# Kernel optimization log

Hardware: AMD Instinct MI355X
Metric: run time of the kernel (lower is better)

The kernel has to match this reference:

```python
import jax, jax.numpy as jnp
import numpy as np

S, N_SUB, E_SUB = 64, 1024, 16384       # subgraphs, nodes/subgraph, edges/subgraph
N, E = 65536, 1048576                   # global nodes / edges
F_IN, NHID, NCLS, HEADS = 128, 128, 64, 2
RATIO = 0.5
K = int(np.ceil(RATIO * N_SUB))         # SAGPooling keeps K=512 nodes


def setup_inputs() -> dict:
    key = jax.random.key(0)
    ks = jax.random.split(key, 12)
    def lin(k, i, o):
        return jax.random.normal(k, (i, o), jnp.float32) / np.sqrt(i).astype(np.float32)
    return {
        'sub_x': jax.random.normal(ks[0], (S, N_SUB, F_IN), jnp.float32),
        'sub_edge_index': jax.random.randint(ks[1], (S, 2, E_SUB), 0, N_SUB, jnp.int32),
        'sub_orig_idx': jax.random.randint(ks[2], (S, N_SUB), 0, N, jnp.int32),
        'edge_index': jax.random.randint(ks[3], (2, E), 0, N, jnp.int32),
        'W1': lin(ks[4], F_IN, NHID), 'b1': jnp.zeros((NHID,), jnp.float32),
        'W2': lin(ks[5], NHID, NHID), 'b2': jnp.zeros((NHID,), jnp.float32),
        'Wp': lin(ks[6], NHID, 1), 'bp': jnp.zeros((1,), jnp.float32),
        'Wsc': lin(ks[7], NHID, NHID), 'bsc': jnp.zeros((NHID,), jnp.float32),
        'Wqkv': lin(ks[8], 2 * NHID, 6 * NHID), 'bqkv': jnp.zeros((6 * NHID,), jnp.float32),
        'Wo': lin(ks[9], 2 * NHID, 2 * NHID), 'bo': jnp.zeros((2 * NHID,), jnp.float32),
        'Wf': lin(ks[10], 3 * NHID, NCLS), 'bf': jnp.zeros((NCLS,), jnp.float32),
    }


def gcn(x, src, dst, ew, W, b, n):
    """PyG GCNConv: sym-normalized aggregation with self-loops; ew masks invalid edges."""
    h = x @ W
    deg = jax.ops.segment_sum(ew, dst, num_segments=n) + 1.0  # +1 self-loop
    dinv = jax.lax.rsqrt(deg)
    coef = dinv[src] * dinv[dst] * ew
    agg = jax.ops.segment_sum(h[src] * coef[:, None], dst, num_segments=n)
    return agg + h * (dinv * dinv)[:, None] + b


def _forward(sub_x, W1, b1, W2, b2, Wp, bp, Wsc, bsc, Wqkv, bqkv, Wo, bo, Wf, bf,
             sub_edge_index, sub_orig_idx, edge_index):
    dt = sub_x.dtype

    def cacos(x, ei):  # one subgraph: [N_SUB,F], [2,E_SUB]
        src, dst = ei[0], ei[1]
        ew1 = jnp.ones((E_SUB,), dt)
        x1 = jax.nn.relu(gcn(x, src, dst, ew1, W1, b1, N_SUB))
        x2 = jax.nn.relu(gcn(x1, src, dst, ew1, W2, b2, N_SUB))
        # SAGPooling on x1: GCN scorer -> top-k -> tanh gate
        score = gcn(x1, src, dst, ew1, Wp, bp, N_SUB)[:, 0]
        top_s, perm = jax.lax.top_k(score, K)
        x_pool = x1[perm] * jnp.tanh(top_s)[:, None]
        # remap edges to pooled indexing; invalid edges get weight 0
        pos = jnp.full((N_SUB,), -1, jnp.int32).at[perm].set(jnp.arange(K, dtype=jnp.int32))
        valid = (pos[src] >= 0) & (pos[dst] >= 0)
        psrc = jnp.where(valid, pos[src], 0)
        pdst = jnp.where(valid, pos[dst], 0)
        ew2 = valid.astype(dt)
        emb1 = jnp.concatenate([x_pool.max(0), x_pool.mean(0)])  # [2*NHID]
        x_sub = jax.nn.relu(gcn(x_pool, psrc, pdst, ew2, Wsc, bsc, K))
        emb2 = jnp.concatenate([x_sub.max(0), x_sub.mean(0)])
        return x2, emb1 + emb2

    node_embs, sub_embs = jax.vmap(cacos)(sub_x, sub_edge_index)  # [S,N_SUB,NHID], [S,2*NHID]

    # multi-head self-attention over subgraph embeddings (seq_len = 1 per the torch reshape)
    HD = (2 * NHID) // HEADS
    qkv = (sub_embs @ Wqkv + bqkv).reshape(S, 1, 3, HEADS, HD).transpose(2, 0, 3, 1, 4)
    q, k, v = qkv[0], qkv[1], qkv[2]                      # [S,H,1,HD]
    attn = jax.nn.softmax(jnp.einsum('shqd,shkd->shqk', q, k) / np.sqrt(HD).astype(np.float32), axis=-1)
    o = jnp.einsum('shqk,shkd->shqd', attn, v).transpose(0, 2, 1, 3).reshape(S, 1, 2 * NHID)
    att = (o @ Wo + bo)[:, 0]                             # [S, 2*NHID]

    # scatter-add per-node embeddings + broadcast subgraph embedding into global buffer
    combined = jnp.concatenate(
        [node_embs, jnp.broadcast_to(att[:, None, :], (S, N_SUB, 2 * NHID))], axis=-1)
    global_emb = jnp.zeros((N, 3 * NHID), dt).at[sub_orig_idx.reshape(-1)].add(
        combined.reshape(-1, 3 * NHID))

    logits = gcn(global_emb, edge_index[0], edge_index[1], jnp.ones((E,), dt), Wf, bf, N)
    return jax.nn.log_softmax(logits, axis=-1), global_emb


def reference(sub_x, sub_edge_index, sub_orig_idx, edge_index, W1, b1, W2, b2, Wp, bp,
              Wsc, bsc, Wqkv, bqkv, Wo, bo, Wf, bf):
    return _forward(sub_x, W1, b1, W2, b2, Wp, bp, Wsc, bsc, Wqkv, bqkv, Wo, bo, Wf, bf,
                    sub_edge_index, sub_orig_idx, edge_index)
```

## Files before the change

### kernel.cpp

```cpp
#include <hip/hip_runtime.h>
#include <math.h>

#define S     64
#define NSUB  1024
#define ESUB  16384
#define NG    65536
#define EG    1048576
#define NH    128
#define KSEL  512
#define BCAP  20480

__global__ __launch_bounds__(1024) void k_csr_sub(const int* __restrict__ sei,
        const int* __restrict__ sorig, int* __restrict__ rowptr, int* __restrict__ col,
        float* __restrict__ dinv, int* __restrict__ cntR) {
    int b = blockIdx.x, t = threadIdx.x;
    if (b >= 64) {
        int r = (b - 64) * 1024 + t;
        atomicAdd(&cntR[sorig[r]], 1);
        return;
    }
    __shared__ int sh[1024];
    __shared__ int curL[1024];
    int s = b;
    curL[t] = 0;
    __syncthreads();
    const int* dstp = sei + s * 2 * ESUB + ESUB;
    #pragma unroll
    for (int k = 0; k < 16; k++) atomicAdd(&curL[dstp[k * 1024 + t]], 1);
    __syncthreads();
    int v = curL[t];
    sh[t] = v;
    __syncthreads();
    for (int off = 1; off < 1024; off <<= 1) {
        int add = (t >= off) ? sh[t - off] : 0;
        __syncthreads();
        sh[t] += add;
        __syncthreads();
    }
    int incl = sh[t];
    int excl = incl - v;
    rowptr[s * (NSUB + 1) + t] = excl;
    dinv[s * NSUB + t] = rsqrtf((float)(v + 1));
    if (t == 1023) rowptr[s * (NSUB + 1) + NSUB] = incl;
    curL[t] = s * ESUB + excl;
    __syncthreads();
    const int* srcp = sei + s * 2 * ESUB;
    #pragma unroll
    for (int k = 0; k < 16; k++) {
        int e = k * 1024 + t;
        int src = srcp[e];
        int dst = dstp[e];
        int p = atomicAdd(&curL[dst], 1);
        col[p] = src;
    }
}

__global__ __launch_bounds__(1024) void k_scanR(const int* __restrict__ cnt,
        int* __restrict__ rowptr, int* __restrict__ cur, int* __restrict__ bcur) {
    __shared__ int sh[1024];
    __shared__ int wsum[16];
    __shared__ int sboff;
    int b = blockIdx.x, t = threadIdx.x;
    if (b == 0 && t < 64) bcur[t] = t * BCAP;
    int pre = 0;
    for (int i = t; i < b * 1024; i += 1024) pre += cnt[i];
    #pragma unroll
    for (int o = 32; o > 0; o >>= 1) pre += __shfl_xor(pre, o, 64);
    if ((t & 63) == 0) wsum[t >> 6] = pre;
    __syncthreads();
    if (t == 0) {
        int r = 0;
        #pragma unroll
        for (int i = 0; i < 16; i++) r += wsum[i];
        sboff = r;
    }
    int v = cnt[b * 1024 + t];
    sh[t] = v;
    __syncthreads();
    for (int off = 1; off < 1024; off <<= 1) {
        int add = (t >= off) ? sh[t - off] : 0;
        __syncthreads();
        sh[t] += add;
        __syncthreads();
    }
    int base = sboff;
    int r = base + sh[t] - v;
    int idx = b * 1024 + t;
    rowptr[idx] = r;
    cur[idx] = r;
    if (b == 63 && t == 1023) rowptr[NG] = base + sh[t];
}

__global__ void k_fillR(const int* __restrict__ orig, int* __restrict__ cur,
                        int* __restrict__ rowlist, int* __restrict__ posR) {
    int r = blockIdx.x * 256 + threadIdx.x;
    int p = atomicAdd(&cur[orig[r]], 1);
    rowlist[p] = r;
    posR[r] = p;
}

template<int KDIM, int NCOL>
__global__ __launch_bounds__(256) void k_matmul(const float* __restrict__ X,
        const float* __restrict__ W, float* __restrict__ Y) {
    __shared__ float As[16][72];
    __shared__ float Bs[16][72];
    int t = threadIdx.x;
    int row0 = blockIdx.x * 64;
    int col0 = blockIdx.y * 64;
    int tr = t >> 4, tc = t & 15;
    float acc[4][4] = {};
    for (int k0 = 0; k0 < KDIM; k0 += 16) {
        {
            int r = t >> 2, kq = t & 3;
            float4 v = *(const float4*)&X[(size_t)(row0 + r) * KDIM + k0 + kq * 4];
            As[kq * 4 + 0][r] = v.x; As[kq * 4 + 1][r] = v.y;
            As[kq * 4 + 2][r] = v.z; As[kq * 4 + 3][r] = v.w;
        }
        {
            int k = t >> 4, cq = t & 15;
            float4 v = *(const float4*)&W[(size_t)(k0 + k) * NCOL + col0 + cq * 4];
            *(float4*)&Bs[k][cq * 4] = v;
        }
        __syncthreads();
        #pragma unroll
        for (int k = 0; k < 16; k++) {
            float a0 = As[k][tr * 4 + 0], a1 = As[k][tr * 4 + 1];
            float a2 = As[k][tr * 4 + 2], a3 = As[k][tr * 4 + 3];
            float b0 = Bs[k][tc * 4 + 0], b1 = Bs[k][tc * 4 + 1];
            float b2 = Bs[k][tc * 4 + 2], b3 = Bs[k][tc * 4 + 3];
            acc[0][0] += a0 * b0; acc[0][1] += a0 * b1; acc[0][2] += a0 * b2; acc[0][3] += a0 * b3;
            acc[1][0] += a1 * b0; acc[1][1] += a1 * b1; acc[1][2] += a1 * b2; acc[1][3] += a1 * b3;
            acc[2][0] += a2 * b0; acc[2][1] += a2 * b1; acc[2][2] += a2 * b2; acc[2][3] += a2 * b3;
            acc[3][0] += a3 * b0; acc[3][1] += a3 * b1; acc[3][2] += a3 * b2; acc[3][3] += a3 * b3;
        }
        __syncthreads();
    }
    #pragma unroll
    for (int i = 0; i < 4; i++) {
        float4 v = { acc[i][0], acc[i][1], acc[i][2], acc[i][3] };
        *(float4*)&Y[(size_t)(row0 + tr * 4 + i) * NCOL + col0 + tc * 4] = v;
    }
}

template<bool SCORE, bool SCATTER>
__global__ __launch_bounds__(256) void k_agg128(const float4* __restrict__ h,
        const float* __restrict__ dinv, const int* __restrict__ rowptr,
        const int* __restrict__ col, const float* __restrict__ bias,
        const float* __restrict__ Wp, const int* __restrict__ posR,
        float4* __restrict__ out, float* __restrict__ scoreh) {
    int b = blockIdx.x;
    int s = b & 63;
    int chunk = b >> 6;
    int t = threadIdx.x;
    int nl = chunk * 8 + (t >> 5);
    int f4 = t & 31;
    const int* rp = rowptr + s * (NSUB + 1);
    int st = rp[nl], en = rp[nl + 1];
    const int* cl = col + s * ESUB;
    const float* dv = dinv + s * NSUB;
    float4 acc = {0.f, 0.f, 0.f, 0.f};
    for (int p = st; p < en; p++) {
        int src = cl[p];
        float d = dv[src];
        float4 hv = h[((size_t)(s * NSUB + src)) * 32 + f4];
        acc.x += hv.x * d; acc.y += hv.y * d; acc.z += hv.z * d; acc.w += hv.w * d;
    }
    size_t node = (size_t)s * NSUB + nl;
    float dn = dv[nl];
    float dn2 = dn * dn;
    float4 hs = h[node * 32 + f4];
    float4 bb = ((const float4*)bias)[f4];
    float4 r;
    r.x = fmaxf(acc.x * dn + hs.x * dn2 + bb.x, 0.f);
    r.y = fmaxf(acc.y * dn + hs.y * dn2 + bb.y, 0.f);
    r.z = fmaxf(acc.z * dn + hs.z * dn2 + bb.z, 0.f);
    r.w = fmaxf(acc.w * dn + hs.w * dn2 + bb.w, 0.f);
    size_t orow = SCATTER ? (size_t)posR[node] : node;
    out[orow * 32 + f4] = r;
    if (SCORE) {
        float4 wp = ((const float4*)Wp)[f4];
        float p = r.x * wp.x + r.y * wp.y + r.z * wp.z + r.w * wp.w;
        #pragma unroll
        for (int o = 16; o > 0; o >>= 1) p += __shfl_xor(p, o, 32);
        if (f4 == 0) scoreh[node] = p;
    }
}

__global__ void k_score_agg(const float* __restrict__ sh, const float* __restrict__ dinv,
                            const int* __restrict__ rowptr, const int* __restrict__ col,
                            const float* __restrict__ bp, float* __restrict__ score) {
    int n = blockIdx.x * 256 + threadIdx.x;
    int s = n >> 10, nl = n & (NSUB - 1);
    const int* rp = rowptr + s * (NSUB + 1);
    const int* cl = col + s * ESUB;
    const float* dv = dinv + s * NSUB;
    int st = rp[nl], en = rp[nl + 1];
    float acc = 0.f;
    for (int p = st; p < en; p++) {
        int src = cl[p];
        acc += sh[s * NSUB + src] * dv[src];
    }
    float dn = dv[nl];
    score[n] = acc * dn + sh[n] * dn * dn + bp[0];
}

__global__ __launch_bounds__(512) void k_topk(const float* __restrict__ score,
        int* __restrict__ perm, float* __restrict__ gate, int* __restrict__ posmap) {
    __shared__ float sv[1024];
    __shared__ int   si[1024];
    int s = blockIdx.x, t = threadIdx.x;
    for (int i = t; i < 1024; i += 512) {
        sv[i] = score[s * NSUB + i];
        si[i] = i;
        posmap[s * NSUB + i] = -1;
    }
    __syncthreads();
    for (int k = 2; k <= 1024; k <<= 1) {
        for (int j = k >> 1; j > 0; j >>= 1) {
            for (int b = t; b < 1024; b += 512) {
                int ixj = b ^ j;
                if (ixj > b) {
                    bool desc = ((b & k) == 0);
                    bool sw = desc ? (sv[b] < sv[ixj]) : (sv[b] > sv[ixj]);
                    if (sw) {
                        float tv = sv[b]; sv[b] = sv[ixj]; sv[ixj] = tv;
                        int ti = si[b]; si[b] = si[ixj]; si[ixj] = ti;
                    }
                }
            }
            __syncthreads();
        }
    }
    if (t < KSEL) {
        perm[s * KSEL + t] = si[t];
        gate[s * KSEL + t] = tanhf(sv[t]);
        posmap[s * NSUB + si[t]] = t;
    }
}

__global__ __launch_bounds__(256) void k_pool(const float4* __restrict__ x1,
        const int* __restrict__ perm, const float* __restrict__ gate,
        const int* __restrict__ posmap, const int* __restrict__ rowptr,
        const int* __restrict__ col, float* __restrict__ dinv2,
        float4* __restrict__ xpool) {
    int t = threadIdx.x;
    int i = blockIdx.x * 8 + (t >> 5);
    int lane = t & 31;
    int s = i >> 9;
    int n = perm[i];
    const int* rp = rowptr + s * (NSUB + 1);
    const int* cl = col + s * ESUB;
    int st = rp[n], en = rp[n + 1];
    int c = 0;
    for (int p = st + lane; p < en; p += 32) c += (posmap[s * NSUB + cl[p]] >= 0) ? 1 : 0;
    #pragma unroll
    for (int o = 16; o > 0; o >>= 1) c += __shfl_xor(c, o, 32);
    if (lane == 0) dinv2[i] = rsqrtf((float)(c + 1));
    float g = gate[i];
    float4 v = x1[((size_t)(s * NSUB + n)) * 32 + lane];
    v.x *= g; v.y *= g; v.z *= g; v.w *= g;
    xpool[(size_t)i * 32 + lane] = v;
}

__global__ __launch_bounds__(1024) void k_emb(const float* __restrict__ X,
        float* __restrict__ out) {
    __shared__ float red[4][256];
    int s = blockIdx.x, t = threadIdx.x;
    int sl = t >> 8, f = t & 255;
    const float* base = X + (size_t)s * KSEL * NH;
    float r;
    if (f < NH) {
        r = -INFINITY;
        for (int i = sl * 128; i < sl * 128 + 128; i++) r = fmaxf(r, base[i * NH + f]);
    } else {
        r = 0.f;
        for (int i = sl * 128; i < sl * 128 + 128; i++) r += base[i * NH + (f - NH)];
    }
    red[sl][f] = r;
    __syncthreads();
    if (sl == 0) {
        float a = red[0][f], b = red[1][f], c = red[2][f], d = red[3][f];
        float v = (f < NH) ? fmaxf(fmaxf(a, b), fmaxf(c, d)) : (a + b + c + d) * (1.f / KSEL);
        out[s * 256 + f] = v;
    }
}

__global__ __launch_bounds__(1024) void k_emb_attn(const float* __restrict__ X,
        const float* __restrict__ subemb, const float* __restrict__ Wqkv,
        const float* __restrict__ bqkv, const float* __restrict__ Wo,
        const float* __restrict__ bo, const float* __restrict__ Wf,
        float* __restrict__ att, float* __restrict__ AW) {
    __shared__ float red[4][256];
    __shared__ float se[256], t1[256], av[256];
    int s = blockIdx.x, t = threadIdx.x;
    int sl = t >> 8, f = t & 255;
    const float* base = X + (size_t)s * KSEL * NH;
    float r;
    if (f < NH) {
        r = -INFINITY;
        for (int i = sl * 128; i < sl * 128 + 128; i++) r = fmaxf(r, base[i * NH + f]);
    } else {
        r = 0.f;
        for (int i = sl * 128; i < sl * 128 + 128; i++) r += base[i * NH + (f - NH)];
    }
    red[sl][f] = r;
    __syncthreads();
    if (sl == 0) {
        float a = red[0][f], b = red[1][f], c = red[2][f], d = red[3][f];
        float v = (f < NH) ? fmaxf(fmaxf(a, b), fmaxf(c, d)) : (a + b + c + d) * (1.f / KSEL);
        se[f] = subemb[s * 256 + f] + v;
    }
    __syncthreads();
    if (sl == 0) {
        float acc = bqkv[512 + f];
        for (int k = 0; k < 256; k++) acc += se[k] * Wqkv[(size_t)k * 768 + 512 + f];
        t1[f] = acc;
    }
    __syncthreads();
    if (sl == 0) {
        float a2 = bo[f];
        for (int k = 0; k < 256; k++) a2 += t1[k] * Wo[(size_t)k * 256 + f];
        att[s * 256 + f] = a2;
        av[f] = a2;
    }
    __syncthreads();
    if (sl == 0 && f < 64) {
        float acc = 0.f;
        for (int k = 0; k < 256; k++) acc += av[k] * Wf[(size_t)(NH + k) * 64 + f];
        AW[s * 64 + f] = acc;
    }
}

__global__ __launch_bounds__(256) void k_agg_pool(const float4* __restrict__ hp,
        const float* __restrict__ dinv2, const int* __restrict__ perm,
        const int* __restrict__ posmap, const int* __restrict__ rowptr,
        const int* __restrict__ col, const float* __restrict__ bsc,
        float4* __restrict__ xsub) {
    int b = blockIdx.x;
    int s = b & 63;
    int chunk = b >> 6;
    int t = threadIdx.x;
    int il = chunk * 8 + (t >> 5);
    int f4 = t & 31;
    int i = s * KSEL + il;
    int n = perm[i];
    const int* rp = rowptr + s * (NSUB + 1);
    const int* cl = col + s * ESUB;
    int st = rp[n], en = rp[n + 1];
    float4 acc = {0.f, 0.f, 0.f, 0.f};
    for (int p = st; p < en; p++) {
        int j = posmap[s * NSUB + cl[p]];
        if (j >= 0) {
            float d = dinv2[s * KSEL + j];
            float4 hv = hp[((size_t)(s * KSEL + j)) * 32 + f4];
            acc.x += hv.x * d; acc.y += hv.y * d; acc.z += hv.z * d; acc.w += hv.w * d;
        }
    }
    float dn = dinv2[i];
    float dn2 = dn * dn;
    float4 hs = hp[(size_t)i * 32 + f4];
    float4 bb = ((const float4*)bsc)[f4];
    float4 r;
    r.x = fmaxf(acc.x * dn + hs.x * dn2 + bb.x, 0.f);
    r.y = fmaxf(acc.y * dn + hs.y * dn2 + bb.y, 0.f);
    r.z = fmaxf(acc.z * dn + hs.z * dn2 + bb.z, 0.f);
    r.w = fmaxf(acc.w * dn + hs.w * dn2 + bb.w, 0.f);
    xsub[(size_t)i * 32 + f4] = r;
}

__global__ __launch_bounds__(384) void k_gather(const float4* __restrict__ x2s,
        const float4* __restrict__ att, const int* __restrict__ rowptrR,
        const int* __restrict__ rowlist, float4* __restrict__ gemb) {
    int t = threadIdx.x;
    int g = blockIdx.x * 4 + (t / 96);
    int lane = t % 96;
    int st = rowptrR[g], en = rowptrR[g + 1];
    float4 acc = {0.f, 0.f, 0.f, 0.f};
    if (lane < 32) {
        for (int p = st; p < en; p++) {
            float4 v = x2s[(size_t)p * 32 + lane];
            acc.x += v.x; acc.y += v.y; acc.z += v.z; acc.w += v.w;
        }
    } else {
        for (int p = st; p < en; p++) {
            int sub = rowlist[p] >> 10;
            float4 v = att[(size_t)sub * 64 + (lane - 32)];
            acc.x += v.x; acc.y += v.y; acc.z += v.z; acc.w += v.w;
        }
    }
    gemb[(size_t)g * 96 + lane] = acc;
}

__global__ __launch_bounds__(256) void k_x2w(const float* __restrict__ X,
        const float* __restrict__ W, const int* __restrict__ rowlist,
        const float* __restrict__ AW, float* __restrict__ Y) {
    __shared__ float As[16][72];
    __shared__ float Bs[16][72];
    int t = threadIdx.x;
    int row0 = blockIdx.x * 64;
    int tr = t >> 4, tc = t & 15;
    float acc[4][4] = {};
    for (int k0 = 0; k0 < 128; k0 += 16) {
        {   int r = t >> 2, kq = t & 3;
            float4 v = *(const float4*)&X[(size_t)(row0 + r) * 128 + k0 + kq * 4];
            As[kq * 4 + 0][r] = v.x; As[kq * 4 + 1][r] = v.y;
            As[kq * 4 + 2][r] = v.z; As[kq * 4 + 3][r] = v.w;
        }
        {   int k = t >> 4, cq = t & 15;
            float4 v = *(const float4*)&W[(size_t)(k0 + k) * 64 + cq * 4];
            *(float4*)&Bs[k][cq * 4] = v;
        }
        __syncthreads();
        #pragma unroll
        for (int k = 0; k < 16; k++) {
            float a0 = As[k][tr * 4 + 0], a1 = As[k][tr * 4 + 1];
            float a2 = As[k][tr * 4 + 2], a3 = As[k][tr * 4 + 3];
            float b0 = Bs[k][tc * 4 + 0], b1 = Bs[k][tc * 4 + 1];
            float b2 = Bs[k][tc * 4 + 2], b3 = Bs[k][tc * 4 + 3];
            acc[0][0] += a0 * b0; acc[0][1] += a0 * b1; acc[0][2] += a0 * b2; acc[0][3] += a0 * b3;
            acc[1][0] += a1 * b0; acc[1][1] += a1 * b1; acc[1][2] += a1 * b2; acc[1][3] += a1 * b3;
            acc[2][0] += a2 * b0; acc[2][1] += a2 * b1; acc[2][2] += a2 * b2; acc[2][3] += a2 * b3;
            acc[3][0] += a3 * b0; acc[3][1] += a3 * b1; acc[3][2] += a3 * b2; acc[3][3] += a3 * b3;
        }
        __syncthreads();
    }
    #pragma unroll
    for (int i = 0; i < 4; i++) {
        int rr = row0 + tr * 4 + i;
        int sub = rowlist[rr] >> 10;
        const float4 aw = *(const float4*)&AW[(size_t)sub * 64 + tc * 4];
        float4 v = { acc[i][0] + aw.x, acc[i][1] + aw.y, acc[i][2] + aw.z, acc[i][3] + aw.w };
        *(float4*)&Y[(size_t)rr * 64 + tc * 4] = v;
    }
}

__global__ __launch_bounds__(256) void k_gatherH(const float4* __restrict__ X2Ws,
        const int* __restrict__ rowptrR, float4* __restrict__ hf) {
    int t = threadIdx.x;
    int g = blockIdx.x * 16 + (t >> 4);
    int f4 = t & 15;
    int st = rowptrR[g], en = rowptrR[g + 1];
    float4 acc = {0.f, 0.f, 0.f, 0.f};
    for (int p = st; p < en; p++) {
        float4 a = X2Ws[(size_t)p * 16 + f4];
        acc.x += a.x; acc.y += a.y; acc.z += a.z; acc.w += a.w;
    }
    hf[(size_t)g * 16 + f4] = acc;
}

__global__ __launch_bounds__(256) void k_binN(const int* __restrict__ gei,
        int* __restrict__ bcur, int* __restrict__ ebin) {
    __shared__ int lh[64];
    __shared__ int lbase[64];
    int t = threadIdx.x;
    if (t < 64) lh[t] = 0;
    __syncthreads();
    int e0 = blockIdx.x * 8192;
    #pragma unroll 8
    for (int k = 0; k < 32; k++) {
        int d = gei[EG + e0 + k * 256 + t];
        atomicAdd(&lh[d >> 10], 1);
    }
    __syncthreads();
    if (t < 64) {
        lbase[t] = atomicAdd(&bcur[t], lh[t]);
        lh[t] = 0;
    }
    __syncthreads();
    #pragma unroll 4
    for (int k = 0; k < 32; k++) {
        int idx = e0 + k * 256 + t;
        int d = gei[EG + idx];
        int src = gei[idx];
        int bb = d >> 10;
        int pos = lbase[bb] + atomicAdd(&lh[bb], 1);
        ebin[pos] = src | ((d & 1023) << 16);
    }
}

__global__ __launch_bounds__(1024) void k_fillB3(const int* __restrict__ ebin,
        const int* __restrict__ bcur, int* __restrict__ rowptrN,
        float* __restrict__ dinvN, int* __restrict__ colN) {
    __shared__ int sh[1024];
    __shared__ int curL[1024];
    __shared__ int sbase;
    int b = blockIdx.x, t = threadIdx.x;
    if (t == 0) {
        int run = 0;
        for (int i = 0; i < b; i++) run += bcur[i] - i * BCAP;
        sbase = run;
    }
    curL[t] = 0;
    __syncthreads();
    int st = b * BCAP, en = bcur[b];
    for (int i = st + t; i < en; i += 1024) atomicAdd(&curL[ebin[i] >> 16], 1);
    __syncthreads();
    int v = curL[t];
    sh[t] = v;
    __syncthreads();
    for (int off = 1; off < 1024; off <<= 1) {
        int add = (t >= off) ? sh[t - off] : 0;
        __syncthreads();
        sh[t] += add;
        __syncthreads();
    }
    int incl = sh[t];
    int excl = incl - v;
    int base = sbase;
    rowptrN[(b << 10) + t] = base + excl;
    dinvN[(b << 10) + t] = rsqrtf((float)(v + 1));
    if (b == 63 && t == 1023) rowptrN[NG] = base + incl;
    curL[t] = base + excl;
    __syncthreads();
    for (int i = st + t; i < en; i += 1024) {
        int packed = ebin[i];
        int p = atomicAdd(&curL[packed >> 16], 1);
        colN[p] = packed & 0xFFFF;
    }
}

__global__ __launch_bounds__(256) void k_final(const float4* __restrict__ hf,
        const float* __restrict__ dinvN, const int* __restrict__ rowptr,
        const int* __restrict__ col, const float* __restrict__ bfb,
        float4* __restrict__ out) {
    int t = threadIdx.x;
    int n = blockIdx.x * 16 + (t >> 4);
    int f4 = t & 15;
    int st = rowptr[n], en = rowptr[n + 1];
    float4 acc = {0.f, 0.f, 0.f, 0.f};
    for (int p = st; p < en; p++) {
        int src = col[p];
        float d = dinvN[src];
        float4 hv = hf[(size_t)src * 16 + f4];
        acc.x += hv.x * d; acc.y += hv.y * d; acc.z += hv.z * d; acc.w += hv.w * d;
    }
    float dn = dinvN[n];
    float dn2 = dn * dn;
    float4 hs = hf[(size_t)n * 16 + f4];
    float4 bb = ((const float4*)bfb)[f4];
    float4 x;
    x.x = acc.x * dn + hs.x * dn2 + bb.x;
    x.y = acc.y * dn + hs.y * dn2 + bb.y;
    x.z = acc.z * dn + hs.z * dn2 + bb.z;
    x.w = acc.w * dn + hs.w * dn2 + bb.w;
    float m = fmaxf(fmaxf(x.x, x.y), fmaxf(x.z, x.w));
    for (int o = 1; o < 16; o <<= 1) m = fmaxf(m, __shfl_xor(m, o, 64));
    float ssum = expf(x.x - m) + expf(x.y - m) + expf(x.z - m) + expf(x.w - m);
    for (int o = 1; o < 16; o <<= 1) ssum += __shfl_xor(ssum, o, 64);
    float lz = m + logf(ssum);
    float4 r = { x.x - lz, x.y - lz, x.z - lz, x.w - lz };
    out[(size_t)n * 16 + f4] = r;
}

extern "C" void kernel_launch(void* const* d_in, const int* in_sizes, int n_in,
                              void* d_out, int out_size, void* d_ws, size_t ws_size,
                              hipStream_t stream) {
    const float* sub_x = (const float*)d_in[0];
    const int*   sei   = (const int*)d_in[1];
    const int*   sorig = (const int*)d_in[2];
    const int*   gei   = (const int*)d_in[3];
    const float *W1 = (const float*)d_in[4],  *b1  = (const float*)d_in[5];
    const float *W2 = (const float*)d_in[6],  *b2  = (const float*)d_in[7];
    const float *Wp = (const float*)d_in[8],  *bp  = (const float*)d_in[9];
    const float *Wsc = (const float*)d_in[10], *bsc = (const float*)d_in[11];
    const float *Wqkv = (const float*)d_in[12], *bqkv = (const float*)d_in[13];
    const float *Wo = (const float*)d_in[14], *bo  = (const float*)d_in[15];
    const float *Wf = (const float*)d_in[16], *bfb = (const float*)d_in[17];

    float* out0 = (float*)d_out;
    float* gemb = (float*)d_out + (size_t)NG * 64;

    char* w = (char*)d_ws;
    size_t off = 0;
    auto alloc = [&](size_t nbytes) -> void* {
        off = (off + 255) & ~(size_t)255;
        void* p = w + off;
        off += nbytes;
        return p;
    };
    int*   bcur    = (int*)alloc(64 * 4);
    float* AW      = (float*)alloc((size_t)S * 64 * 4);
    float* dinv    = (float*)alloc((size_t)NG * 4);
    float* scoreh  = (float*)alloc((size_t)NG * 4);
    float* score   = (float*)alloc((size_t)NG * 4);
    float* gate    = (float*)alloc((size_t)S * KSEL * 4);
    float* dinv2   = (float*)alloc((size_t)S * KSEL * 4);
    float* subemb  = (float*)alloc((size_t)S * 256 * 4);
    float* att     = (float*)alloc((size_t)S * 256 * 4);
    int*   perm    = (int*)alloc((size_t)S * KSEL * 4);
    int*   posmap  = (int*)alloc((size_t)NG * 4);
    int*   cur_sub = (int*)alloc((size_t)NG * 4);
    int*   rowptr_s= (int*)alloc((size_t)(NG + 64) * 4);
    int*   col_sub = (int*)alloc((size_t)EG * 4);
    int*   rowptrR = (int*)alloc((size_t)(NG + 64) * 4);
    int*   cntR    = (int*)alloc((size_t)NG * 4);
    int*   rowlist = (int*)alloc((size_t)NG * 4);
    int*   posR    = (int*)alloc((size_t)NG * 4);
    float* x1      = (float*)alloc((size_t)NG * NH * 4);
    float* x2s     = (float*)alloc((size_t)NG * NH * 4);
    float* hbuf    = (float*)alloc((size_t)NG * NH * 4);
    float* xpool   = (float*)alloc((size_t)S * KSEL * NH * 4);
    float* xsub    = x1;
    float* hf      = hbuf;
    float* dinvN   = dinv;
    float* X2Ws    = x1;
    int*   curR    = cur_sub;
    int*   rowptrN = rowptr_s;
    int*   colN    = col_sub;
    int*   ebin    = (int*)xpool;

    hipMemsetAsync(cntR, 0, (size_t)NG * 4, stream);

    k_csr_sub<<<128, 1024, 0, stream>>>(sei, sorig, rowptr_s, col_sub, dinv, cntR);
    k_scanR<<<64, 1024, 0, stream>>>(cntR, rowptrR, curR, bcur);
    k_fillR<<<NG / 256, 256, 0, stream>>>(sorig, curR, rowlist, posR);

    k_matmul<128, 128><<<dim3(NG / 64, 2), 256, 0, stream>>>(sub_x, W1, hbuf);
    k_agg128<true, false><<<8192, 256, 0, stream>>>((const float4*)hbuf, dinv, rowptr_s,
                                                    col_sub, b1, Wp, nullptr, (float4*)x1, scoreh);
    k_matmul<128, 128><<<dim3(NG / 64, 2), 256, 0, stream>>>(x1, W2, hbuf);
    k_agg128<false, true><<<8192, 256, 0, stream>>>((const float4*)hbuf, dinv, rowptr_s,
                                                    col_sub, b2, nullptr, posR, (float4*)x2s, nullptr);
    k_score_agg<<<NG / 256, 256, 0, stream>>>(scoreh, dinv, rowptr_s, col_sub, bp, score);
    k_topk<<<S, 512, 0, stream>>>(score, perm, gate, posmap);
    k_pool<<<(S * KSEL) / 8, 256, 0, stream>>>((const float4*)x1, perm, gate, posmap,
                                               rowptr_s, col_sub, dinv2, (float4*)xpool);
    k_emb<<<S, 1024, 0, stream>>>(xpool, subemb);
    k_matmul<128, 128><<<dim3((S * KSEL) / 64, 2), 256, 0, stream>>>(xpool, Wsc, hbuf);
    k_agg_pool<<<4096, 256, 0, stream>>>((const float4*)hbuf, dinv2, perm, posmap,
                                         rowptr_s, col_sub, bsc, (float4*)xsub);
    k_emb_attn<<<S, 1024, 0, stream>>>(xsub, subemb, Wqkv, bqkv, Wo, bo, Wf, att, AW);

    k_binN<<<EG / 8192, 256, 0, stream>>>(gei, bcur, ebin);
    k_fillB3<<<64, 1024, 0, stream>>>(ebin, bcur, rowptrN, dinvN, colN);

    k_gather<<<NG / 4, 384, 0, stream>>>((const float4*)x2s, (const float4*)att,
                                         rowptrR, rowlist, (float4*)gemb);
    k_x2w<<<NG / 64, 256, 0, stream>>>(x2s, Wf, rowlist, AW, X2Ws);
    k_gatherH<<<NG / 16, 256, 0, stream>>>((const float4*)X2Ws, rowptrR, (float4*)hf);

    k_final<<<NG / 16, 256, 0, stream>>>((const float4*)hf, dinvN, rowptrN, colN, bfb, (float4*)out0);

    (void)in_sizes; (void)n_in; (void)out_size; (void)ws_size;
}
```

Before: 720.7 us.

## Merge independent kernels into shared launches via block-index partitioning

Several independent kernels are merged into single launches that split work by block index: the layer-2 matmul with score aggregation, pooled aggregation with global edge binning, embedding attention with CSR fill, and gather with the x2·Wf matmul. The bcur counter is now zeroed by the existing memset instead of set by k_scanR, and offsets are computed from counts. This cuts launch count and lets small, low-occupancy kernels overlap with larger ones. In exchange, heterogeneous blocks share one launch configuration, and the gather path is reshaped to 256-thread blocks with one warp handling all three segments.

```diff
diff --git a/kernel.cpp b/kernel.cpp
--- a/kernel.cpp
+++ b/kernel.cpp
@@ -56,12 +56,11 @@
 }
 
 __global__ __launch_bounds__(1024) void k_scanR(const int* __restrict__ cnt,
-        int* __restrict__ rowptr, int* __restrict__ cur, int* __restrict__ bcur) {
+        int* __restrict__ rowptr, int* __restrict__ cur) {
     __shared__ int sh[1024];
     __shared__ int wsum[16];
     __shared__ int sboff;
     int b = blockIdx.x, t = threadIdx.x;
-    if (b == 0 && t < 64) bcur[t] = t * BCAP;
     int pre = 0;
     for (int i = t; i < b * 1024; i += 1024) pre += cnt[i];
     #pragma unroll
@@ -110,14 +109,12 @@
     int tr = t >> 4, tc = t & 15;
     float acc[4][4] = {};
     for (int k0 = 0; k0 < KDIM; k0 += 16) {
-        {
-            int r = t >> 2, kq = t & 3;
+        {   int r = t >> 2, kq = t & 3;
             float4 v = *(const float4*)&X[(size_t)(row0 + r) * KDIM + k0 + kq * 4];
             As[kq * 4 + 0][r] = v.x; As[kq * 4 + 1][r] = v.y;
             As[kq * 4 + 2][r] = v.z; As[kq * 4 + 3][r] = v.w;
         }
-        {
-            int k = t >> 4, cq = t & 15;
+        {   int k = t >> 4, cq = t & 15;
             float4 v = *(const float4*)&W[(size_t)(k0 + k) * NCOL + col0 + cq * 4];
             *(float4*)&Bs[k][cq * 4] = v;
         }
@@ -139,6 +136,65 @@
     for (int i = 0; i < 4; i++) {
         float4 v = { acc[i][0], acc[i][1], acc[i][2], acc[i][3] };
         *(float4*)&Y[(size_t)(row0 + tr * 4 + i) * NCOL + col0 + tc * 4] = v;
+    }
+}
+
+__global__ __launch_bounds__(256) void k_mm2s(const float* __restrict__ X,
+        const float* __restrict__ W, float* __restrict__ Y,
+        const float* __restrict__ sh, const float* __restrict__ dinv,
+        const int* __restrict__ rowptr, const int* __restrict__ col,
+        const float* __restrict__ bp, float* __restrict__ score) {
+    int t = threadIdx.x;
+    if (blockIdx.x >= 2048) {
+        int n = (blockIdx.x - 2048) * 256 + t;
+        int s = n >> 10, nl = n & (NSUB - 1);
+        const int* rp = rowptr + s * (NSUB + 1);
+        const int* cl = col + s * ESUB;
+        const float* dv = dinv + s * NSUB;
+        int st = rp[nl], en = rp[nl + 1];
+        float acc = 0.f;
+        for (int p = st; p < en; p++) {
+            int src = cl[p];
+            acc += sh[s * NSUB + src] * dv[src];
+        }
+        float dn = dv[nl];
+        score[n] = acc * dn + sh[n] * dn * dn + bp[0];
+        return;
+    }
+    __shared__ float As[16][72];
+    __shared__ float Bs[16][72];
+    int row0 = (blockIdx.x & 1023) * 64;
+    int col0 = (blockIdx.x >> 10) * 64;
+    int tr = t >> 4, tc = t & 15;
+    float acc[4][4] = {};
+    for (int k0 = 0; k0 < 128; k0 += 16) {
+        {   int r = t >> 2, kq = t & 3;
+            float4 v = *(const float4*)&X[(size_t)(row0 + r) * 128 + k0 + kq * 4];
+            As[kq * 4 + 0][r] = v.x; As[kq * 4 + 1][r] = v.y;
+            As[kq * 4 + 2][r] = v.z; As[kq * 4 + 3][r] = v.w;
+        }
+        {   int k = t >> 4, cq = t & 15;
+            float4 v = *(const float4*)&W[(size_t)(k0 + k) * 128 + col0 + cq * 4];
+            *(float4*)&Bs[k][cq * 4] = v;
+        }
+        __syncthreads();
+        #pragma unroll
+        for (int k = 0; k < 16; k++) {
+            float a0 = As[k][tr * 4 + 0], a1 = As[k][tr * 4 + 1];
+            float a2 = As[k][tr * 4 + 2], a3 = As[k][tr * 4 + 3];
+            float b0 = Bs[k][tc * 4 + 0], b1 = Bs[k][tc * 4 + 1];
+            float b2 = Bs[k][tc * 4 + 2], b3 = Bs[k][tc * 4 + 3];
+            acc[0][0] += a0 * b0; acc[0][1] += a0 * b1; acc[0][2] += a0 * b2; acc[0][3] += a0 * b3;
+            acc[1][0] += a1 * b0; acc[1][1] += a1 * b1; acc[1][2] += a1 * b2; acc[1][3] += a1 * b3;
+            acc[2][0] += a2 * b0; acc[2][1] += a2 * b1; acc[2][2] += a2 * b2; acc[2][3] += a2 * b3;
+            acc[3][0] += a3 * b0; acc[3][1] += a3 * b1; acc[3][2] += a3 * b2; acc[3][3] += a3 * b3;
+        }
+        __syncthreads();
+    }
+    #pragma unroll
+    for (int i = 0; i < 4; i++) {
+        float4 v = { acc[i][0], acc[i][1], acc[i][2], acc[i][3] };
+        *(float4*)&Y[(size_t)(row0 + tr * 4 + i) * 128 + col0 + tc * 4] = v;
     }
 }
 
@@ -186,24 +242,6 @@
     }
 }
 
-__global__ void k_score_agg(const float* __restrict__ sh, const float* __restrict__ dinv,
-                            const int* __restrict__ rowptr, const int* __restrict__ col,
-                            const float* __restrict__ bp, float* __restrict__ score) {
-    int n = blockIdx.x * 256 + threadIdx.x;
-    int s = n >> 10, nl = n & (NSUB - 1);
-    const int* rp = rowptr + s * (NSUB + 1);
-    const int* cl = col + s * ESUB;
-    const float* dv = dinv + s * NSUB;
-    int st = rp[nl], en = rp[nl + 1];
-    float acc = 0.f;
-    for (int p = st; p < en; p++) {
-        int src = cl[p];
-        acc += sh[s * NSUB + src] * dv[src];
-    }
-    float dn = dv[nl];
-    score[n] = acc * dn + sh[n] * dn * dn + bp[0];
-}
-
 __global__ __launch_bounds__(512) void k_topk(const float* __restrict__ score,
         int* __restrict__ perm, float* __restrict__ gate, int* __restrict__ posmap) {
     __shared__ float sv[1024];
@@ -285,61 +323,44 @@
     }
 }
 
-__global__ __launch_bounds__(1024) void k_emb_attn(const float* __restrict__ X,
-        const float* __restrict__ subemb, const float* __restrict__ Wqkv,
-        const float* __restrict__ bqkv, const float* __restrict__ Wo,
-        const float* __restrict__ bo, const float* __restrict__ Wf,
-        float* __restrict__ att, float* __restrict__ AW) {
-    __shared__ float red[4][256];
-    __shared__ float se[256], t1[256], av[256];
-    int s = blockIdx.x, t = threadIdx.x;
-    int sl = t >> 8, f = t & 255;
-    const float* base = X + (size_t)s * KSEL * NH;
-    float r;
-    if (f < NH) {
-        r = -INFINITY;
-        for (int i = sl * 128; i < sl * 128 + 128; i++) r = fmaxf(r, base[i * NH + f]);
-    } else {
-        r = 0.f;
-        for (int i = sl * 128; i < sl * 128 + 128; i++) r += base[i * NH + (f - NH)];
-    }
-    red[sl][f] = r;
-    __syncthreads();
-    if (sl == 0) {
-        float a = red[0][f], b = red[1][f], c = red[2][f], d = red[3][f];
-        float v = (f < NH) ? fmaxf(fmaxf(a, b), fmaxf(c, d)) : (a + b + c + d) * (1.f / KSEL);
-        se[f] = subemb[s * 256 + f] + v;
-    }
-    __syncthreads();
-    if (sl == 0) {
-        float acc = bqkv[512 + f];
-        for (int k = 0; k < 256; k++) acc += se[k] * Wqkv[(size_t)k * 768 + 512 + f];
-        t1[f] = acc;
-    }
-    __syncthreads();
-    if (sl == 0) {
-        float a2 = bo[f];
-        for (int k = 0; k < 256; k++) a2 += t1[k] * Wo[(size_t)k * 256 + f];
-        att[s * 256 + f] = a2;
-        av[f] = a2;
-    }
-    __syncthreads();
-    if (sl == 0 && f < 64) {
-        float acc = 0.f;
-        for (int k = 0; k < 256; k++) acc += av[k] * Wf[(size_t)(NH + k) * 64 + f];
-        AW[s * 64 + f] = acc;
-    }
-}
-
-__global__ __launch_bounds__(256) void k_agg_pool(const float4* __restrict__ hp,
+__global__ __launch_bounds__(256) void k_aggp_bin(const float4* __restrict__ hp,
         const float* __restrict__ dinv2, const int* __restrict__ perm,
         const int* __restrict__ posmap, const int* __restrict__ rowptr,
         const int* __restrict__ col, const float* __restrict__ bsc,
-        float4* __restrict__ xsub) {
+        float4* __restrict__ xsub,
+        const int* __restrict__ gei, int* __restrict__ bcur, int* __restrict__ ebin) {
+    int t = threadIdx.x;
+    if (blockIdx.x >= 4096) {
+        __shared__ int lh[64];
+        __shared__ int lbase[64];
+        if (t < 64) lh[t] = 0;
+        __syncthreads();
+        int e0 = (blockIdx.x - 4096) * 8192;
+        #pragma unroll 8
+        for (int k = 0; k < 32; k++) {
+            int d = gei[EG + e0 + k * 256 + t];
+            atomicAdd(&lh[d >> 10], 1);
+        }
+        __syncthreads();
+        if (t < 64) {
+            lbase[t] = t * BCAP + atomicAdd(&bcur[t], lh[t]);
+            lh[t] = 0;
+        }
+        __syncthreads();
+        #pragma unroll 4
+        for (int k = 0; k < 32; k++) {
+            int idx = e0 + k * 256 + t;
+            int d = gei[EG + idx];
+            int src = gei[idx];
+            int bb = d >> 10;
+            int pos = lbase[bb] + atomicAdd(&lh[bb], 1);
+            ebin[pos] = src | ((d & 1023) << 16);
+        }
+        return;
+    }
     int b = blockIdx.x;
     int s = b & 63;
     int chunk = b >> 6;
-    int t = threadIdx.x;
     int il = chunk * 8 + (t >> 5);
     int f4 = t & 31;
     int i = s * KSEL + il;
@@ -368,36 +389,122 @@
     xsub[(size_t)i * 32 + f4] = r;
 }
 
-__global__ __launch_bounds__(384) void k_gather(const float4* __restrict__ x2s,
+__global__ __launch_bounds__(1024) void k_ea_fb(const float* __restrict__ X,
+        const float* __restrict__ subemb, const float* __restrict__ Wqkv,
+        const float* __restrict__ bqkv, const float* __restrict__ Wo,
+        const float* __restrict__ bo, const float* __restrict__ Wf,
+        float* __restrict__ att, float* __restrict__ AW,
+        const int* __restrict__ ebin, const int* __restrict__ bcur,
+        int* __restrict__ rowptrN, float* __restrict__ dinvN, int* __restrict__ colN) {
+    int t = threadIdx.x;
+    if (blockIdx.x >= 64) {
+        __shared__ int sh2[1024];
+        __shared__ int curL[1024];
+        __shared__ int sbase;
+        int b = blockIdx.x - 64;
+        if (t == 0) {
+            int run = 0;
+            for (int i = 0; i < b; i++) run += bcur[i];
+            sbase = run;
+        }
+        curL[t] = 0;
+        __syncthreads();
+        int st = b * BCAP, en = st + bcur[b];
+        for (int i = st + t; i < en; i += 1024) atomicAdd(&curL[ebin[i] >> 16], 1);
+        __syncthreads();
+        int v = curL[t];
+        sh2[t] = v;
+        __syncthreads();
+        for (int off = 1; off < 1024; off <<= 1) {
+            int add = (t >= off) ? sh2[t - off] : 0;
+            __syncthreads();
+            sh2[t] += add;
+            __syncthreads();
+        }
+        int incl = sh2[t];
+        int excl = incl - v;
+        int base = sbase;
+        rowptrN[(b << 10) + t] = base + excl;
+        dinvN[(b << 10) + t] = rsqrtf((float)(v + 1));
+        if (b == 63 && t == 1023) rowptrN[NG] = base + incl;
+        curL[t] = base + excl;
+        __syncthreads();
+        for (int i = st + t; i < en; i += 1024) {
+            int packed = ebin[i];
+            int p = atomicAdd(&curL[packed >> 16], 1);
+            colN[p] = packed & 0xFFFF;
+        }
+        return;
+    }
+    __shared__ float red[4][256];
+    __shared__ float se[256], t1[256], av[256];
+    int s = blockIdx.x;
+    int sl = t >> 8, f = t & 255;
+    const float* base = X + (size_t)s * KSEL * NH;
+    float r;
+    if (f < NH) {
+        r = -INFINITY;
+        for (int i = sl * 128; i < sl * 128 + 128; i++) r = fmaxf(r, base[i * NH + f]);
+    } else {
+        r = 0.f;
+        for (int i = sl * 128; i < sl * 128 + 128; i++) r += base[i * NH + (f - NH)];
+    }
+    red[sl][f] = r;
+    __syncthreads();
+    if (sl == 0) {
+        float a = red[0][f], b = red[1][f], c = red[2][f], d = red[3][f];
+        float v = (f < NH) ? fmaxf(fmaxf(a, b), fmaxf(c, d)) : (a + b + c + d) * (1.f / KSEL);
+        se[f] = subemb[s * 256 + f] + v;
+    }
+    __syncthreads();
+    if (sl == 0) {
+        float acc = bqkv[512 + f];
+        for (int k = 0; k < 256; k++) acc += se[k] * Wqkv[(size_t)k * 768 + 512 + f];
+        t1[f] = acc;
+    }
+    __syncthreads();
+    if (sl == 0) {
+        float a2 = bo[f];
+        for (int k = 0; k < 256; k++) a2 += t1[k] * Wo[(size_t)k * 256 + f];
+        att[s * 256 + f] = a2;
+        av[f] = a2;
+    }
+    __syncthreads();
+    if (sl == 0 && f < 64) {
+        float acc = 0.f;
+        for (int k = 0; k < 256; k++) acc += av[k] * Wf[(size_t)(NH + k) * 64 + f];
+        AW[s * 64 + f] = acc;
+    }
+}
+
+__global__ __launch_bounds__(256) void k_gx(const float4* __restrict__ x2s,
         const float4* __restrict__ att, const int* __restrict__ rowptrR,
-        const int* __restrict__ rowlist, float4* __restrict__ gemb) {
-    int t = threadIdx.x;
-    int g = blockIdx.x * 4 + (t / 96);
-    int lane = t % 96;
-    int st = rowptrR[g], en = rowptrR[g + 1];
-    float4 acc = {0.f, 0.f, 0.f, 0.f};
-    if (lane < 32) {
+        const int* __restrict__ rowlist, float4* __restrict__ gemb,
+        const float* __restrict__ X, const float* __restrict__ W,
+        const float* __restrict__ AW, float* __restrict__ Y) {
+    int t = threadIdx.x;
+    if (blockIdx.x < NG / 8) {
+        int g = blockIdx.x * 8 + (t >> 5);
+        int lane = t & 31;
+        int st = rowptrR[g], en = rowptrR[g + 1];
+        float4 a0 = {0.f,0.f,0.f,0.f}, a1 = {0.f,0.f,0.f,0.f}, a2 = {0.f,0.f,0.f,0.f};
         for (int p = st; p < en; p++) {
             float4 v = x2s[(size_t)p * 32 + lane];
-            acc.x += v.x; acc.y += v.y; acc.z += v.z; acc.w += v.w;
-        }
-    } else {
-        for (int p = st; p < en; p++) {
+            a0.x += v.x; a0.y += v.y; a0.z += v.z; a0.w += v.w;
             int sub = rowlist[p] >> 10;
-            float4 v = att[(size_t)sub * 64 + (lane - 32)];
-            acc.x += v.x; acc.y += v.y; acc.z += v.z; acc.w += v.w;
-        }
-    }
-    gemb[(size_t)g * 96 + lane] = acc;
-}
-
-__global__ __launch_bounds__(256) void k_x2w(const float* __restrict__ X,
-        const float* __restrict__ W, const int* __restrict__ rowlist,
-        const float* __restrict__ AW, float* __restrict__ Y) {
+            float4 w1 = att[(size_t)sub * 64 + lane];
+            float4 w2 = att[(size_t)sub * 64 + 32 + lane];
+            a1.x += w1.x; a1.y += w1.y; a1.z += w1.z; a1.w += w1.w;
+            a2.x += w2.x; a2.y += w2.y; a2.z += w2.z; a2.w += w2.w;
+        }
+        gemb[(size_t)g * 96 + lane]      = a0;
+        gemb[(size_t)g * 96 + 32 + lane] = a1;
+        gemb[(size_t)g * 96 + 64 + lane] = a2;
+        return;
+    }
     __shared__ float As[16][72];
     __shared__ float Bs[16][72];
-    int t = threadIdx.x;
-    int row0 = blockIdx.x * 64;
+    int row0 = (blockIdx.x - NG / 8) * 64;
     int tr = t >> 4, tc = t & 15;
     float acc[4][4] = {};
     for (int k0 = 0; k0 < 128; k0 += 16) {
@@ -446,77 +553,6 @@
         acc.x += a.x; acc.y += a.y; acc.z += a.z; acc.w += a.w;
     }
     hf[(size_t)g * 16 + f4] = acc;
-}
-
-__global__ __launch_bounds__(256) void k_binN(const int* __restrict__ gei,
-        int* __restrict__ bcur, int* __restrict__ ebin) {
-    __shared__ int lh[64];
-    __shared__ int lbase[64];
-    int t = threadIdx.x;
-    if (t < 64) lh[t] = 0;
-    __syncthreads();
-    int e0 = blockIdx.x * 8192;
-    #pragma unroll 8
-    for (int k = 0; k < 32; k++) {
-        int d = gei[EG + e0 + k * 256 + t];
-        atomicAdd(&lh[d >> 10], 1);
-    }
-    __syncthreads();
-    if (t < 64) {
-        lbase[t] = atomicAdd(&bcur[t], lh[t]);
-        lh[t] = 0;
-    }
-    __syncthreads();
-    #pragma unroll 4
-    for (int k = 0; k < 32; k++) {
-        int idx = e0 + k * 256 + t;
-        int d = gei[EG + idx];
-        int src = gei[idx];
-        int bb = d >> 10;
-        int pos = lbase[bb] + atomicAdd(&lh[bb], 1);
-        ebin[pos] = src | ((d & 1023) << 16);
-    }
-}
-
-__global__ __launch_bounds__(1024) void k_fillB3(const int* __restrict__ ebin,
-        const int* __restrict__ bcur, int* __restrict__ rowptrN,
-        float* __restrict__ dinvN, int* __restrict__ colN) {
-    __shared__ int sh[1024];
-    __shared__ int curL[1024];
-    __shared__ int sbase;
-    int b = blockIdx.x, t = threadIdx.x;
-    if (t == 0) {
-        int run = 0;
-        for (int i = 0; i < b; i++) run += bcur[i] - i * BCAP;
-        sbase = run;
-    }
-    curL[t] = 0;
-    __syncthreads();
-    int st = b * BCAP, en = bcur[b];
-    for (int i = st + t; i < en; i += 1024) atomicAdd(&curL[ebin[i] >> 16], 1);
-    __syncthreads();
-    int v = curL[t];
-    sh[t] = v;
-    __syncthreads();
-    for (int off = 1; off < 1024; off <<= 1) {
-        int add = (t >= off) ? sh[t - off] : 0;
-        __syncthreads();
-        sh[t] += add;
-        __syncthreads();
-    }
-    int incl = sh[t];
-    int excl = incl - v;
-    int base = sbase;
-    rowptrN[(b << 10) + t] = base + excl;
-    dinvN[(b << 10) + t] = rsqrtf((float)(v + 1));
-    if (b == 63 && t == 1023) rowptrN[NG] = base + incl;
-    curL[t] = base + excl;
-    __syncthreads();
-    for (int i = st + t; i < en; i += 1024) {
-        int packed = ebin[i];
-        int p = atomicAdd(&curL[packed >> 16], 1);
-        colN[p] = packed & 0xFFFF;
-    }
 }
 
 __global__ __launch_bounds__(256) void k_final(const float4* __restrict__ hf,
@@ -579,6 +615,7 @@
         return p;
     };
     int*   bcur    = (int*)alloc(64 * 4);
+    int*   cntR    = (int*)alloc((size_t)NG * 4);
     float* AW      = (float*)alloc((size_t)S * 64 * 4);
     float* dinv    = (float*)alloc((size_t)NG * 4);
     float* scoreh  = (float*)alloc((size_t)NG * 4);
@@ -593,7 +630,6 @@
     int*   rowptr_s= (int*)alloc((size_t)(NG + 64) * 4);
     int*   col_sub = (int*)alloc((size_t)EG * 4);
     int*   rowptrR = (int*)alloc((size_t)(NG + 64) * 4);
-    int*   cntR    = (int*)alloc((size_t)NG * 4);
     int*   rowlist = (int*)alloc((size_t)NG * 4);
     int*   posR    = (int*)alloc((size_t)NG * 4);
     float* x1      = (float*)alloc((size_t)NG * NH * 4);
@@ -609,34 +645,32 @@
     int*   colN    = col_sub;
     int*   ebin    = (int*)xpool;
 
-    hipMemsetAsync(cntR, 0, (size_t)NG * 4, stream);
+    hipMemsetAsync(bcur, 0, 256 + (size_t)NG * 4, stream);
 
     k_csr_sub<<<128, 1024, 0, stream>>>(sei, sorig, rowptr_s, col_sub, dinv, cntR);
-    k_scanR<<<64, 1024, 0, stream>>>(cntR, rowptrR, curR, bcur);
+    k_scanR<<<64, 1024, 0, stream>>>(cntR, rowptrR, curR);
     k_fillR<<<NG / 256, 256, 0, stream>>>(sorig, curR, rowlist, posR);
 
     k_matmul<128, 128><<<dim3(NG / 64, 2), 256, 0, stream>>>(sub_x, W1, hbuf);
     k_agg128<true, false><<<8192, 256, 0, stream>>>((const float4*)hbuf, dinv, rowptr_s,
                                                     col_sub, b1, Wp, nullptr, (float4*)x1, scoreh);
-    k_matmul<128, 128><<<dim3(NG / 64, 2), 256, 0, stream>>>(x1, W2, hbuf);
+    k_mm2s<<<2048 + NG / 256, 256, 0, stream>>>(x1, W2, hbuf,
+                                                scoreh, dinv, rowptr_s, col_sub, bp, score);
     k_agg128<false, true><<<8192, 256, 0, stream>>>((const float4*)hbuf, dinv, rowptr_s,
                                                     col_sub, b2, nullptr, posR, (float4*)x2s, nullptr);
-    k_score_agg<<<NG / 256, 256, 0, stream>>>(scoreh, dinv, rowptr_s, col_sub, bp, score);
     k_topk<<<S, 512, 0, stream>>>(score, perm, gate, posmap);
     k_pool<<<(S * KSEL) / 8, 256, 0, stream>>>((const float4*)x1, perm, gate, posmap,
                                                rowptr_s, col_sub, dinv2, (float4*)xpool);
     k_emb<<<S, 1024, 0, stream>>>(xpool, subemb);
     k_matmul<128, 128><<<dim3((S * KSEL) / 64, 2), 256, 0, stream>>>(xpool, Wsc, hbuf);
-    k_agg_pool<<<4096, 256, 0, stream>>>((const float4*)hbuf, dinv2, perm, posmap,
-                                         rowptr_s, col_sub, bsc, (float4*)xsub);
-    k_emb_attn<<<S, 1024, 0, stream>>>(xsub, subemb, Wqkv, bqkv, Wo, bo, Wf, att, AW);
-
-    k_binN<<<EG / 8192, 256, 0, stream>>>(gei, bcur, ebin);
-    k_fillB3<<<64, 1024, 0, stream>>>(ebin, bcur, rowptrN, dinvN, colN);
-
-    k_gather<<<NG / 4, 384, 0, stream>>>((const float4*)x2s, (const float4*)att,
-                                         rowptrR, rowlist, (float4*)gemb);
-    k_x2w<<<NG / 64, 256, 0, stream>>>(x2s, Wf, rowlist, AW, X2Ws);
+    k_aggp_bin<<<4096 + EG / 8192, 256, 0, stream>>>((const float4*)hbuf, dinv2, perm, posmap,
+                                                     rowptr_s, col_sub, bsc, (float4*)xsub,
+                                                     gei, bcur, ebin);
+    k_ea_fb<<<128, 1024, 0, stream>>>(xsub, subemb, Wqkv, bqkv, Wo, bo, Wf, att, AW,
+                                      ebin, bcur, rowptrN, dinvN, colN);
+    k_gx<<<NG / 8 + NG / 64, 256, 0, stream>>>((const float4*)x2s, (const float4*)att,
+                                               rowptrR, rowlist, (float4*)gemb,
+                                               x2s, Wf, AW, X2Ws);
     k_gatherH<<<NG / 16, 256, 0, stream>>>((const float4*)X2Ws, rowptrR, (float4*)hf);
 
     k_final<<<NG / 16, 256, 0, stream>>>((const float4*)hf, dinvN, rowptrN, colN, bfb, (float4*)out0);
```

New measurement: 682.1 us. -5.4%, faster.
